# Optimization experiments

Measured on AMD Instinct MI355X. Metric: run time of the kernel, lower is better.

The kernel has to match this reference:

```python
import jax, jax.numpy as jnp
import numpy as np

EPS = 1e-6

def _ln(x, g, b):
    m = jnp.mean(x, axis=-1, keepdims=True)
    v = jnp.mean(jnp.square(x - m), axis=-1, keepdims=True)
    return (x - m) / jnp.sqrt(v + EPS) * g + b

def setup_inputs() -> dict:
    key = jax.random.key(0)
    ks = jax.random.split(key, 16)
    B, L, D = 4, 2048, 1024
    s = 0.02
    inp = {
        'q': jax.random.normal(ks[0], (B, L, D), jnp.float32),
        'k': jax.random.normal(ks[1], (B, L, D), jnp.float32),
        'v': jax.random.normal(ks[2], (B, L, D), jnp.float32),
    }
    wnames = ['Wq1', 'Wk1', 'Wv1', 'Wf1', 'Wq2', 'Wk2', 'Wv2', 'Wf2']
    for i, n in enumerate(wnames):
        inp[n] = jax.random.normal(ks[3 + i], (D, D), jnp.float32) * s
        inp['b' + n[1:]] = jnp.zeros((D,), jnp.float32)
    for n in ['q1', 'k1', 'v1', 'q2', 'k2', 'v2']:
        inp['g' + n] = jnp.ones((D,), jnp.float32)
        inp['B' + n] = jnp.zeros((D,), jnp.float32)
    return inp

def reference(q, k, v, Wq1, bq1, Wk1, bk1, Wv1, bv1, Wf1, bf1,
              Wq2, bq2, Wk2, bk2, Wv2, bv2, Wf2, bf2,
              gq1, Bq1, gk1, Bk1, gv1, Bv1, gq2, Bq2, gk2, Bk2, gv2, Bv2):
    # n_head = 1 (forced by LayerNorm(n_head*d_k) on last dim d_k); d_k = 1024
    temp = jnp.sqrt(jnp.asarray(q.shape[-1], q.dtype))

    def attn(qi, ki, vi):
        a = jax.nn.softmax(jnp.einsum('bqd,bkd->bqk', qi / temp, ki), axis=-1)
        return jnp.einsum('bqk,bkd->bqd', a, vi), a

    # layer 1
    q1 = q @ Wq1 + bq1
    k1 = k @ Wk1 + bk1
    v1 = v @ Wv1 + bv1
    residual1 = q1
    o1, _ = attn(_ln(q1, gq1, Bq1), _ln(k1, gk1, Bk1), _ln(v1, gv1, Bv1))
    o1 = o1 @ Wf1 + bf1
    # layer 2
    q2 = o1 @ Wq2 + bq2
    k2 = k @ Wk2 + bk2
    v2 = v @ Wv2 + bv2
    residual2 = q2
    o2, a2 = attn(_ln(q2, gq2, Bq2), _ln(k2, gk2, Bk2), _ln(v2, gv2, Bv2))
    out = o2 @ Wf2 + bf2
    # residuals in torch have shape (b, l, 1, d_k); cat on last dim -> (b, l, 1, 2*d_k)
    res = jnp.concatenate([residual1, residual2], axis=-1)[:, :, None, :]
    # attn2.squeeze() drops the singleton head dim -> (b, lq, lk)
    return out, res, a2
```

## Files before the change

### kernel.cpp

```cpp
#include <hip/hip_runtime.h>

#define DEV __device__ __forceinline__

using short8  = __attribute__((ext_vector_type(8))) short;
using floatx4 = __attribute__((ext_vector_type(4))) float;

DEV unsigned short f2bf(float f) {
  unsigned int u = __float_as_uint(f);
  u += 0x7FFFu + ((u >> 16) & 1u);
  return (unsigned short)(u >> 16);
}
DEV float bf2f(unsigned short u) { return __uint_as_float(((unsigned int)u) << 16); }

DEV void stage16(void* lds, const void* g) {
  __builtin_amdgcn_global_load_lds(
      (__attribute__((address_space(1))) void*)g,
      (__attribute__((address_space(3))) void*)lds, 16, 0, 0);
}

DEV float wave_sum(float x) {
#pragma unroll
  for (int m = 32; m; m >>= 1) x += __shfl_xor(x, m);
  return x;
}
DEV float wave_max(float x) {
#pragma unroll
  for (int m = 32; m; m >>= 1) x = fmaxf(x, __shfl_xor(x, m));
  return x;
}

DEV void gemm_core(const short* __restrict__ A, const short* __restrict__ Bt,
                   const float* __restrict__ bias,
                   float* __restrict__ Cf, unsigned short* __restrict__ Cb,
                   float* __restrict__ C2, int offc2,
                   int N, int K, int m0, int n0) {
  __shared__ __align__(16) short As[128 * 32];
  __shared__ __align__(16) short Bs[128 * 32];

  const int t    = threadIdx.x;
  const int lane = t & 63;
  const int w    = t >> 6;
  const int wr   = (w >> 1) * 64;
  const int wc   = (w & 1) * 64;
  const int mr   = lane & 15;
  const int kq   = lane >> 4;
  const int ca   = kq ^ ((mr >> 1) & 3);

  floatx4 acc[4][4];
#pragma unroll
  for (int i = 0; i < 4; ++i)
#pragma unroll
    for (int j = 0; j < 4; ++j)
      acc[i][j] = (floatx4){0.f, 0.f, 0.f, 0.f};

  for (int k0 = 0; k0 < K; k0 += 32) {
#pragma unroll
    for (int i = 0; i < 2; ++i) {
      const int c   = t + i * 256;
      const int row = c >> 2;
      const int cc  = c & 3;
      const int sc  = cc ^ ((row >> 1) & 3);
      stage16(&As[c * 8], A  + (size_t)(m0 + row) * K + k0 + sc * 8);
      stage16(&Bs[c * 8], Bt + (size_t)(n0 + row) * K + k0 + sc * 8);
    }
    __syncthreads();

    short8 af[4], bf4[4];
#pragma unroll
    for (int i = 0; i < 4; ++i)
      af[i] = *(const short8*)&As[(wr + i * 16 + mr) * 32 + ca * 8];
#pragma unroll
    for (int j = 0; j < 4; ++j)
      bf4[j] = *(const short8*)&Bs[(wc + j * 16 + mr) * 32 + ca * 8];
#pragma unroll
    for (int i = 0; i < 4; ++i)
#pragma unroll
      for (int j = 0; j < 4; ++j)
        acc[i][j] = __builtin_amdgcn_mfma_f32_16x16x32_bf16(af[i], bf4[j], acc[i][j], 0, 0, 0);
    __syncthreads();
  }

#pragma unroll
  for (int i = 0; i < 4; ++i) {
#pragma unroll
    for (int r = 0; r < 4; ++r) {
      const int row = m0 + wr + i * 16 + kq * 4 + r;
#pragma unroll
      for (int j = 0; j < 4; ++j) {
        const int col = n0 + wc + j * 16 + mr;
        float vv = acc[i][j][r];
        if (bias) vv += bias[col];
        if (Cf) Cf[(size_t)row * N + col] = vv;
        if (Cb) Cb[(size_t)row * N + col] = f2bf(vv);
        if (C2) C2[(size_t)row * 2048 + offc2 + col] = vv;
      }
    }
  }
}

__global__ __launch_bounds__(256)
void gemm_bt(const short* __restrict__ A, long long sAz,
             const short* __restrict__ Bt, long long sBz,
             const float* __restrict__ bias,
             float* __restrict__ Cf, long long sCfz,
             unsigned short* __restrict__ Cb, long long sCbz,
             float* __restrict__ C2, int offc2,
             int N, int K) {
  const int z = blockIdx.z;
  gemm_core(A + (long long)z * sAz, Bt + (long long)z * sBz, bias,
            Cf ? Cf + (long long)z * sCfz : (float*)0,
            Cb ? Cb + (long long)z * sCbz : (unsigned short*)0,
            C2, offc2, N, K, blockIdx.y * 128, blockIdx.x * 128);
}

struct ProjJob {
  const short* A;
  const short* Bt;
  const float* bias;
  unsigned short* Cb;
  float* C2;
  long long offc2;
};
struct Proj5 { ProjJob j[5]; };

__global__ __launch_bounds__(256)
void gemm_proj5(Proj5 p) {
  ProjJob jb = p.j[0];
#pragma unroll
  for (int i = 1; i < 5; ++i)
    if ((int)blockIdx.z == i) jb = p.j[i];
  gemm_core(jb.A, jb.Bt, jb.bias, (float*)0, jb.Cb, jb.C2, (int)jb.offc2,
            1024, 1024, blockIdx.y * 128, blockIdx.x * 128);
}

struct LnJob {
  const unsigned short* x;
  const float* bias;
  const float* g;
  const float* Bb;
  unsigned short* y;
  float scale;
};

__global__ __launch_bounds__(256)
void ln_multi(LnJob j0, LnJob j1, LnJob j2, LnJob j3, LnJob j4) {
  LnJob jb = j0;
  if (blockIdx.y == 1) jb = j1;
  else if (blockIdx.y == 2) jb = j2;
  else if (blockIdx.y == 3) jb = j3;
  else if (blockIdx.y == 4) jb = j4;
  const int row = blockIdx.x, t = threadIdx.x;
  const ushort4 xv = ((const ushort4*)(jb.x + (size_t)row * 1024))[t];
  float4 v = {bf2f(xv.x), bf2f(xv.y), bf2f(xv.z), bf2f(xv.w)};
  if (jb.bias) {
    const float4 b4 = ((const float4*)jb.bias)[t];
    v.x += b4.x; v.y += b4.y; v.z += b4.z; v.w += b4.w;
  }
  float s  = v.x + v.y + v.z + v.w;
  float s2 = v.x * v.x + v.y * v.y + v.z * v.z + v.w * v.w;
  s = wave_sum(s);
  s2 = wave_sum(s2);
  __shared__ float r1[4], r2[4];
  const int w = t >> 6, lane = t & 63;
  if (!lane) { r1[w] = s; r2[w] = s2; }
  __syncthreads();
  s  = r1[0] + r1[1] + r1[2] + r1[3];
  s2 = r2[0] + r2[1] + r2[2] + r2[3];
  const float mean = s * (1.f / 1024.f);
  const float var  = s2 * (1.f / 1024.f) - mean * mean;
  const float rstd = 1.f / sqrtf(var + 1e-6f);
  const float4 g4 = ((const float4*)jb.g)[t];
  const float4 b4 = ((const float4*)jb.Bb)[t];
  ushort4 o;
  o.x = f2bf(((v.x - mean) * rstd * g4.x + b4.x) * jb.scale);
  o.y = f2bf(((v.y - mean) * rstd * g4.y + b4.y) * jb.scale);
  o.z = f2bf(((v.z - mean) * rstd * g4.z + b4.z) * jb.scale);
  o.w = f2bf(((v.w - mean) * rstd * g4.w + b4.w) * jb.scale);
  ((ushort4*)(jb.y + (size_t)row * 1024))[t] = o;
}

__global__ __launch_bounds__(256)
void softmax_kernel(const float* __restrict__ S, unsigned short* __restrict__ P,
                    float* __restrict__ A2) {
  const int row = blockIdx.x, t = threadIdx.x;
  const float4* sr = (const float4*)(S + (size_t)row * 2048);
  float4 a = sr[t], b = sr[t + 256];
  float m = fmaxf(fmaxf(fmaxf(a.x, a.y), fmaxf(a.z, a.w)),
                  fmaxf(fmaxf(b.x, b.y), fmaxf(b.z, b.w)));
  m = wave_max(m);
  __shared__ float red[4];
  const int w = t >> 6, lane = t & 63;
  if (!lane) red[w] = m;
  __syncthreads();
  m = fmaxf(fmaxf(red[0], red[1]), fmaxf(red[2], red[3]));
  a.x = __expf(a.x - m); a.y = __expf(a.y - m); a.z = __expf(a.z - m); a.w = __expf(a.w - m);
  b.x = __expf(b.x - m); b.y = __expf(b.y - m); b.z = __expf(b.z - m); b.w = __expf(b.w - m);
  float s = a.x + a.y + a.z + a.w + b.x + b.y + b.z + b.w;
  s = wave_sum(s);
  __syncthreads();
  if (!lane) red[w] = s;
  __syncthreads();
  s = red[0] + red[1] + red[2] + red[3];
  const float inv = 1.f / s;
  a.x *= inv; a.y *= inv; a.z *= inv; a.w *= inv;
  b.x *= inv; b.y *= inv; b.z *= inv; b.w *= inv;
  ushort4 o0, o1;
  o0.x = f2bf(a.x); o0.y = f2bf(a.y); o0.z = f2bf(a.z); o0.w = f2bf(a.w);
  o1.x = f2bf(b.x); o1.y = f2bf(b.y); o1.z = f2bf(b.z); o1.w = f2bf(b.w);
  ((ushort4*)(P + (size_t)row * 2048))[t] = o0;
  ((ushort4*)(P + (size_t)row * 2048))[t + 256] = o1;
  if (A2) {
    float4* ar = (float4*)(A2 + (size_t)row * 2048);
    ar[t] = a;
    ar[t + 256] = b;
  }
}

__global__ __launch_bounds__(256)
void cast3_kernel(const float* __restrict__ x0, const float* __restrict__ x1,
                  const float* __restrict__ x2, unsigned short* __restrict__ y0,
                  unsigned short* __restrict__ y1, unsigned short* __restrict__ y2) {
  const float* x = blockIdx.y == 0 ? x0 : (blockIdx.y == 1 ? x1 : x2);
  unsigned short* y = blockIdx.y == 0 ? y0 : (blockIdx.y == 1 ? y1 : y2);
  const int i = blockIdx.x * 256 + threadIdx.x;
  const float4 v = ((const float4*)x)[i];
  ushort4 o;
  o.x = f2bf(v.x); o.y = f2bf(v.y); o.z = f2bf(v.z); o.w = f2bf(v.w);
  ((ushort4*)y)[i] = o;
}

struct W8 {
  const float* src[8];
  unsigned short* dst[8];
};

__global__ __launch_bounds__(256)
void transpose_w8_kernel(W8 p) {
  __shared__ unsigned short tile[64][65];
  const float* in = p.src[blockIdx.z];
  unsigned short* out = p.dst[blockIdx.z];
  const int tr0 = blockIdx.y * 64, tc0 = blockIdx.x * 64;
  const int x = threadIdx.x & 63, y = threadIdx.x >> 6;
#pragma unroll
  for (int i = 0; i < 16; ++i) {
    const int r = i * 4 + y;
    tile[r][x] = f2bf(in[(size_t)(tr0 + r) * 1024 + tc0 + x]);
  }
  __syncthreads();
#pragma unroll
  for (int i = 0; i < 16; ++i) {
    const int r = i * 4 + y;
    out[(size_t)(tc0 + r) * 1024 + tr0 + x] = tile[x][r];
  }
}

__global__ __launch_bounds__(256)
void transpose_v8_kernel(const unsigned short* __restrict__ in0,
                         const unsigned short* __restrict__ in1,
                         unsigned short* __restrict__ out0,
                         unsigned short* __restrict__ out1) {
  __shared__ unsigned short tile[64][65];
  const int zz = blockIdx.z & 3;
  const unsigned short* in = (blockIdx.z < 4 ? in0 : in1) + (size_t)zz * 2048 * 1024;
  unsigned short* out = (blockIdx.z < 4 ? out0 : out1) + (size_t)zz * 1024 * 2048;
  const int tr0 = blockIdx.y * 64, tc0 = blockIdx.x * 64;
  const int x = threadIdx.x & 63, y = threadIdx.x >> 6;
#pragma unroll
  for (int i = 0; i < 16; ++i) {
    const int r = i * 4 + y;
    tile[r][x] = in[(size_t)(tr0 + r) * 1024 + tc0 + x];
  }
  __syncthreads();
#pragma unroll
  for (int i = 0; i < 16; ++i) {
    const int r = i * 4 + y;
    out[(size_t)(tc0 + r) * 2048 + tr0 + x] = tile[x][r];
  }
}

extern "C" void kernel_launch(void* const* d_in, const int* in_sizes, int n_in,
                              void* d_out, int out_size, void* d_ws, size_t ws_size,
                              hipStream_t stream) {
  const float* q = (const float*)d_in[0];
  const float* k = (const float*)d_in[1];
  const float* v = (const float*)d_in[2];
  const float* W[8];
  const float* bW[8];
  for (int i = 0; i < 8; ++i) {
    W[i]  = (const float*)d_in[3 + 2 * i];
    bW[i] = (const float*)d_in[4 + 2 * i];
  }
  const float* g_[6];
  const float* B_[6];
  for (int i = 0; i < 6; ++i) {
    g_[i] = (const float*)d_in[19 + 2 * i];
    B_[i] = (const float*)d_in[20 + 2 * i];
  }

  float* out_p = (float*)d_out;
  float* res_p = out_p + 8388608;
  float* a2_p  = res_p + 16777216;

  char* ws = (char*)d_ws;
  const size_t MBy = 1u << 20;
  unsigned short* WT   = (unsigned short*)ws;
  unsigned short* qb   = (unsigned short*)(ws + 16 * MBy);
  unsigned short* kb   = (unsigned short*)(ws + 32 * MBy);
  unsigned short* vb   = (unsigned short*)(ws + 48 * MBy);
  unsigned short* pb   = (unsigned short*)(ws + 64 * MBy);
  float* Sbuf          = (float*)(ws + 64 * MBy);
  unsigned short* lnq  = (unsigned short*)(ws + 144 * MBy);
  unsigned short* lnk1 = (unsigned short*)(ws + 160 * MBy);
  unsigned short* lnk2 = (unsigned short*)(ws + 176 * MBy);
  unsigned short* lnv1 = (unsigned short*)(ws + 192 * MBy);
  unsigned short* lnv2 = (unsigned short*)(ws + 208 * MBy);
  unsigned short* lnvT1= (unsigned short*)(ws + 224 * MBy);
  unsigned short* lnvT2= (unsigned short*)(ws + 240 * MBy);
  unsigned short* P    = (unsigned short*)(ws + 256 * MBy);
  unsigned short* ofb  = (unsigned short*)(ws + 290 * MBy);
  unsigned short* ob   = (unsigned short*)(ws + 306 * MBy);
  unsigned short* qf2b = (unsigned short*)(ws + 322 * MBy);

  const size_t SL = 8192ull * 1024;

  auto gemm = [&](const unsigned short* A, long long sAz,
                  const unsigned short* Bt, long long sBz, const float* bias,
                  float* Cf, long long sCfz, unsigned short* Cb, long long sCbz,
                  float* C2, int offc2, int M, int N, int K, int Z) {
    dim3 grid(N / 128, M / 128, Z);
    gemm_bt<<<grid, 256, 0, stream>>>((const short*)A, sAz, (const short*)Bt, sBz,
                                      bias, Cf, sCfz, Cb, sCbz, C2, offc2, N, K);
  };
  LnJob nil{};

  cast3_kernel<<<dim3(8192, 3), 256, 0, stream>>>(q, k, v, qb, kb, vb);
  W8 w8;
  for (int i = 0; i < 8; ++i) { w8.src[i] = W[i]; w8.dst[i] = WT + (size_t)i * 1048576; }
  transpose_w8_kernel<<<dim3(16, 16, 8), 256, 0, stream>>>(w8);

  {
    Proj5 p;
    p.j[0] = {(const short*)kb, (const short*)(WT + 1u * 1048576), 0, pb + 0 * SL, 0, 0};
    p.j[1] = {(const short*)kb, (const short*)(WT + 5u * 1048576), 0, pb + 1 * SL, 0, 0};
    p.j[2] = {(const short*)vb, (const short*)(WT + 2u * 1048576), 0, pb + 2 * SL, 0, 0};
    p.j[3] = {(const short*)vb, (const short*)(WT + 6u * 1048576), 0, pb + 3 * SL, 0, 0};
    p.j[4] = {(const short*)qb, (const short*)(WT + 0u * 1048576), bW[0], pb + 4 * SL, res_p, 0};
    gemm_proj5<<<dim3(8, 64, 5), 256, 0, stream>>>(p);
  }

  {
    LnJob jk1{pb + 0 * SL, bW[1], g_[1], B_[1], lnk1, 1.f};
    LnJob jk2{pb + 1 * SL, bW[5], g_[4], B_[4], lnk2, 1.f};
    LnJob jv1{pb + 2 * SL, bW[2], g_[2], B_[2], lnv1, 1.f};
    LnJob jv2{pb + 3 * SL, bW[6], g_[5], B_[5], lnv2, 1.f};
    LnJob jq1{pb + 4 * SL, 0,     g_[0], B_[0], lnq,  1.f / 32.f};
    ln_multi<<<dim3(8192, 5), 256, 0, stream>>>(jk1, jk2, jv1, jv2, jq1);
  }
  transpose_v8_kernel<<<dim3(16, 32, 8), 256, 0, stream>>>(lnv1, lnv2, lnvT1, lnvT2);

  gemm(lnq, 2048ll * 1024, lnk1, 2048ll * 1024, 0, Sbuf, 2048ll * 2048, 0, 0, 0, 0,
       2048, 2048, 1024, 4);
  softmax_kernel<<<8192, 256, 0, stream>>>(Sbuf, P, (float*)0);
  gemm(P, 2048ll * 2048, lnvT1, 1024ll * 2048, 0, 0, 0, ob, 2048ll * 1024, 0, 0,
       2048, 1024, 2048, 4);
  gemm(ob, 0, WT + 3u * 1048576, 0, bW[3], 0, 0, ofb, 0, 0, 0, 8192, 1024, 1024, 1);

  gemm(ofb, 0, WT + 4u * 1048576, 0, bW[4], 0, 0, qf2b, 0, res_p, 1024, 8192, 1024, 1024, 1);
  {
    LnJob jq2{qf2b, 0, g_[3], B_[3], lnq, 1.f / 32.f};
    ln_multi<<<dim3(8192, 1), 256, 0, stream>>>(jq2, nil, nil, nil, nil);
  }
  gemm(lnq, 2048ll * 1024, lnk2, 2048ll * 1024, 0, Sbuf, 2048ll * 2048, 0, 0, 0, 0,
       2048, 2048, 1024, 4);
  softmax_kernel<<<8192, 256, 0, stream>>>(Sbuf, P, a2_p);
  gemm(P, 2048ll * 2048, lnvT2, 1024ll * 2048, 0, 0, 0, ob, 2048ll * 1024, 0, 0,
       2048, 1024, 2048, 4);
  gemm(ob, 0, WT + 7u * 1048576, 0, bW[7], out_p, 0, 0, 0, 0, 0, 8192, 1024, 1024, 1);
}
```

Before: 978.5 us.

## Pipeline GEMM with 4-stage LDS ring buffer and XCD-aware block remapping

Replaces the single-buffered GEMM mainloop, which synchronized twice per k-step, with a 4-slot LDS ring. Tiles are prefetched three steps ahead via global_load_lds, with manual vmcnt waits and one barrier per iteration. Each wave now stages either A or B rows with a new swizzle, and MFMA issue is wrapped in s_setprio. Block IDs are also remapped so consecutive tiles land on the same XCD for better L2 locality. The cost is 64KB of LDS per block, which may reduce occupancy, plus hand-written wait counts that must stay correct.

```diff
diff --git a/kernel.cpp b/kernel.cpp
--- a/kernel.cpp
+++ b/kernel.cpp
@@ -29,22 +29,37 @@
   return x;
 }
 
-DEV void gemm_core(const short* __restrict__ A, const short* __restrict__ Bt,
+DEV void g128_core(const short* __restrict__ A, const short* __restrict__ Bt,
                    const float* __restrict__ bias,
                    float* __restrict__ Cf, unsigned short* __restrict__ Cb,
                    float* __restrict__ C2, int offc2,
                    int N, int K, int m0, int n0) {
-  __shared__ __align__(16) short As[128 * 32];
-  __shared__ __align__(16) short Bs[128 * 32];
+  __shared__ __align__(16) short lds[4][8192];
 
   const int t    = threadIdx.x;
   const int lane = t & 63;
   const int w    = t >> 6;
-  const int wr   = (w >> 1) * 64;
-  const int wc   = (w & 1) * 64;
-  const int mr   = lane & 15;
-  const int kq   = lane >> 4;
-  const int ca   = kq ^ ((mr >> 1) & 3);
+  const int wm   = w >> 1;
+  const int wn   = w & 1;
+  const int NT   = K >> 5;
+
+  const int isB  = w >> 1;
+  const int row0 = (isB ? n0 : m0) + (w & 1) * 64 + (lane >> 2);
+  const int csw  = ((lane & 3) * 8) ^ ((lane >> 5) << 4);
+  const short* gbase = isB ? Bt : A;
+  const short* gp[4];
+#pragma unroll
+  for (int i = 0; i < 4; ++i)
+    gp[i] = gbase + (size_t)(row0 + i * 16) * K + csw;
+  const int ldst = isB * 4096 + (w & 1) * 2048 + lane * 8;
+
+  auto stage = [&](int tt) {
+    short* dst = &lds[tt & 3][ldst];
+    const int go = tt * 32;
+#pragma unroll
+    for (int i = 0; i < 4; ++i)
+      stage16(dst + i * 512, gp[i] + go);
+  };
 
   floatx4 acc[4][4];
 #pragma unroll
@@ -53,42 +68,48 @@
     for (int j = 0; j < 4; ++j)
       acc[i][j] = (floatx4){0.f, 0.f, 0.f, 0.f};
 
-  for (int k0 = 0; k0 < K; k0 += 32) {
-#pragma unroll
-    for (int i = 0; i < 2; ++i) {
-      const int c   = t + i * 256;
-      const int row = c >> 2;
-      const int cc  = c & 3;
-      const int sc  = cc ^ ((row >> 1) & 3);
-      stage16(&As[c * 8], A  + (size_t)(m0 + row) * K + k0 + sc * 8);
-      stage16(&Bs[c * 8], Bt + (size_t)(n0 + row) * K + k0 + sc * 8);
-    }
-    __syncthreads();
-
-    short8 af[4], bf4[4];
-#pragma unroll
-    for (int i = 0; i < 4; ++i)
-      af[i] = *(const short8*)&As[(wr + i * 16 + mr) * 32 + ca * 8];
-#pragma unroll
-    for (int j = 0; j < 4; ++j)
-      bf4[j] = *(const short8*)&Bs[(wc + j * 16 + mr) * 32 + ca * 8];
-#pragma unroll
-    for (int i = 0; i < 4; ++i)
-#pragma unroll
-      for (int j = 0; j < 4; ++j)
-        acc[i][j] = __builtin_amdgcn_mfma_f32_16x16x32_bf16(af[i], bf4[j], acc[i][j], 0, 0, 0);
-    __syncthreads();
-  }
-
-#pragma unroll
-  for (int i = 0; i < 4; ++i) {
+  stage(0); stage(1); stage(2);
+
+  const int mr = lane & 15, q = lane >> 4;
+  const int fo = mr * 32 + ((q * 8) ^ ((mr & 8) << 1));
+
+  for (int kt = 0; kt < NT; ++kt) {
+    asm volatile("s_waitcnt lgkmcnt(0)" ::: "memory");
+    const int rem = NT - 1 - kt;
+    if (rem >= 2)      asm volatile("s_waitcnt vmcnt(8)" ::: "memory");
+    else if (rem == 1) asm volatile("s_waitcnt vmcnt(4)" ::: "memory");
+    else               asm volatile("s_waitcnt vmcnt(0)" ::: "memory");
+    __builtin_amdgcn_s_barrier();
+    __builtin_amdgcn_sched_barrier(0);
+
+    if (kt + 3 < NT) stage(kt + 3);
+
+    const short* bufA = &lds[kt & 3][wm * 2048];
+    const short* bufB = &lds[kt & 3][4096 + wn * 2048];
+    short8 a[4], b[4];
+#pragma unroll
+    for (int m = 0; m < 4; ++m) a[m] = *(const short8*)&bufA[m * 512 + fo];
+#pragma unroll
+    for (int n = 0; n < 4; ++n) b[n] = *(const short8*)&bufB[n * 512 + fo];
+
+    __builtin_amdgcn_s_setprio(1);
+#pragma unroll
+    for (int m = 0; m < 4; ++m)
+#pragma unroll
+      for (int n = 0; n < 4; ++n)
+        acc[m][n] = __builtin_amdgcn_mfma_f32_16x16x32_bf16(a[m], b[n], acc[m][n], 0, 0, 0);
+    __builtin_amdgcn_s_setprio(0);
+  }
+
+#pragma unroll
+  for (int m = 0; m < 4; ++m) {
 #pragma unroll
     for (int r = 0; r < 4; ++r) {
-      const int row = m0 + wr + i * 16 + kq * 4 + r;
-#pragma unroll
-      for (int j = 0; j < 4; ++j) {
-        const int col = n0 + wc + j * 16 + mr;
-        float vv = acc[i][j][r];
+      const int row = m0 + wm * 64 + m * 16 + q * 4 + r;
+#pragma unroll
+      for (int n = 0; n < 4; ++n) {
+        const int col = n0 + wn * 64 + n * 16 + mr;
+        float vv = acc[m][n][r];
         if (bias) vv += bias[col];
         if (Cf) Cf[(size_t)row * N + col] = vv;
         if (Cb) Cb[(size_t)row * N + col] = f2bf(vv);
@@ -98,19 +119,32 @@
   }
 }
 
-__global__ __launch_bounds__(256)
-void gemm_bt(const short* __restrict__ A, long long sAz,
+DEV void xcd_decode(int gx, int gy, int& bx, int& by, int& bz) {
+  const int nwg = gx * gy * gridDim.z;
+  int bid = ((int)blockIdx.z * gy + (int)blockIdx.y) * gx + (int)blockIdx.x;
+  const int qq = nwg >> 3, rr = nwg & 7;
+  const int xcd = bid & 7, jj = bid >> 3;
+  bid = (xcd < rr ? xcd * (qq + 1) : rr * (qq + 1) + (xcd - rr) * qq) + jj;
+  bx = bid % gx;
+  const int tmp = bid / gx;
+  by = tmp % gy;
+  bz = tmp / gy;
+}
+
+__global__ __launch_bounds__(256)
+void g128_bt(const short* __restrict__ A, long long sAz,
              const short* __restrict__ Bt, long long sBz,
              const float* __restrict__ bias,
              float* __restrict__ Cf, long long sCfz,
              unsigned short* __restrict__ Cb, long long sCbz,
              float* __restrict__ C2, int offc2,
              int N, int K) {
-  const int z = blockIdx.z;
-  gemm_core(A + (long long)z * sAz, Bt + (long long)z * sBz, bias,
-            Cf ? Cf + (long long)z * sCfz : (float*)0,
-            Cb ? Cb + (long long)z * sCbz : (unsigned short*)0,
-            C2, offc2, N, K, blockIdx.y * 128, blockIdx.x * 128);
+  int bx, by, bz;
+  xcd_decode(gridDim.x, gridDim.y, bx, by, bz);
+  g128_core(A + (long long)bz * sAz, Bt + (long long)bz * sBz, bias,
+            Cf ? Cf + (long long)bz * sCfz : (float*)0,
+            Cb ? Cb + (long long)bz * sCbz : (unsigned short*)0,
+            C2, offc2, N, K, by * 128, bx * 128);
 }
 
 struct ProjJob {
@@ -124,13 +158,15 @@
 struct Proj5 { ProjJob j[5]; };
 
 __global__ __launch_bounds__(256)
-void gemm_proj5(Proj5 p) {
+void g128_proj5(Proj5 p) {
+  int bx, by, bz;
+  xcd_decode(gridDim.x, gridDim.y, bx, by, bz);
   ProjJob jb = p.j[0];
 #pragma unroll
   for (int i = 1; i < 5; ++i)
-    if ((int)blockIdx.z == i) jb = p.j[i];
-  gemm_core(jb.A, jb.Bt, jb.bias, (float*)0, jb.Cb, jb.C2, (int)jb.offc2,
-            1024, 1024, blockIdx.y * 128, blockIdx.x * 128);
+    if (bz == i) jb = p.j[i];
+  g128_core(jb.A, jb.Bt, jb.bias, (float*)0, jb.Cb, jb.C2, (int)jb.offc2,
+            1024, 1024, by * 128, bx * 128);
 }
 
 struct LnJob {
@@ -328,7 +364,7 @@
                   float* Cf, long long sCfz, unsigned short* Cb, long long sCbz,
                   float* C2, int offc2, int M, int N, int K, int Z) {
     dim3 grid(N / 128, M / 128, Z);
-    gemm_bt<<<grid, 256, 0, stream>>>((const short*)A, sAz, (const short*)Bt, sBz,
+    g128_bt<<<grid, 256, 0, stream>>>((const short*)A, sAz, (const short*)Bt, sBz,
                                       bias, Cf, sCfz, Cb, sCbz, C2, offc2, N, K);
   };
   LnJob nil{};
@@ -345,7 +381,7 @@
     p.j[2] = {(const short*)vb, (const short*)(WT + 2u * 1048576), 0, pb + 2 * SL, 0, 0};
     p.j[3] = {(const short*)vb, (const short*)(WT + 6u * 1048576), 0, pb + 3 * SL, 0, 0};
     p.j[4] = {(const short*)qb, (const short*)(WT + 0u * 1048576), bW[0], pb + 4 * SL, res_p, 0};
-    gemm_proj5<<<dim3(8, 64, 5), 256, 0, stream>>>(p);
+    g128_proj5<<<dim3(8, 64, 5), 256, 0, stream>>>(p);
   }
 
   {
```

Result: faster. 862.8 us (-11.8%).
